# Kernel tuning notes

Hardware: AMD Instinct MI355X
Metric: run time of the kernel (lower is better)

## Reference

```python
import jax, jax.numpy as jnp
import numpy as np

N_NODES = 50000
NEG_SLOPE = 0.2


def _gat_conv(x, src, dst, W, a_src, a_dst, b, num_nodes):
    # W: [H*C, F_in]; a_src/a_dst: [H, C]; b: [H*C]
    H, C = a_src.shape
    xp = (x @ W.T).reshape(num_nodes, H, C)              # [N,H,C]
    alpha_s = jnp.sum(xp * a_src[None], axis=-1)          # [N,H]
    alpha_d = jnp.sum(xp * a_dst[None], axis=-1)          # [N,H]
    e = jax.nn.leaky_relu(alpha_s[src] + alpha_d[dst], NEG_SLOPE)  # [E,H]
    # segment softmax over incoming edges of each dst node (self-loops guarantee non-empty segments)
    m = jax.ops.segment_max(e, dst, num_segments=num_nodes)
    e = jnp.exp(e - m[dst])
    s = jax.ops.segment_sum(e, dst, num_segments=num_nodes)
    alpha = e / s[dst]                                    # [E,H]
    out = jax.ops.segment_sum(alpha[:, :, None] * xp[src], dst, num_segments=num_nodes)  # [N,H,C]
    return out.reshape(num_nodes, H * C) + b


def setup_inputs() -> dict:
    key = jax.random.key(0)
    ks = jax.random.split(key, 12)
    N, E, F_in, HID, H, Z = N_NODES, 800000, 128, 64, 2, 32
    sc = 0.1
    return {
        "features": jax.random.normal(ks[0], (N, F_in), jnp.float32),
        "edges": jax.random.randint(ks[1], (2, E), 0, N, jnp.int32),
        "W1": jax.random.normal(ks[2], (H * HID, F_in), jnp.float32) * sc,
        "a_src1": jax.random.normal(ks[3], (H, HID), jnp.float32) * sc,
        "a_dst1": jax.random.normal(ks[4], (H, HID), jnp.float32) * sc,
        "b1": jnp.zeros((H * HID,), jnp.float32),
        "W_mu": jax.random.normal(ks[5], (Z, H * HID), jnp.float32) * sc,
        "a_src_mu": jax.random.normal(ks[6], (1, Z), jnp.float32) * sc,
        "a_dst_mu": jax.random.normal(ks[7], (1, Z), jnp.float32) * sc,
        "b_mu": jnp.zeros((Z,), jnp.float32),
        "W_std": jax.random.normal(ks[8], (Z, H * HID), jnp.float32) * sc,
        "a_src_std": jax.random.normal(ks[9], (1, Z), jnp.float32) * sc,
        "a_dst_std": jax.random.normal(ks[10], (1, Z), jnp.float32) * sc,
        "b_std": jnp.zeros((Z,), jnp.float32),
    }


def reference(features, edges, W1, a_src1, a_dst1, b1, W_mu, a_src_mu, a_dst_mu, b_mu, W_std, a_src_std, a_dst_std, b_std):
    N = features.shape[0]
    loops = jnp.arange(N, dtype=edges.dtype)
    src = jnp.concatenate([edges[0], loops])  # add self loops (PyG default)
    dst = jnp.concatenate([edges[1], loops])
    h = _gat_conv(features, src, dst, W1, a_src1, a_dst1, b1, N)
    h = jax.nn.relu(h)  # dropout p=0.0 -> identity
    mu = _gat_conv(h, src, dst, W_mu, a_src_mu, a_dst_mu, b_mu, N)
    std = _gat_conv(h, src, dst, W_std, a_src_std, a_dst_std, b_std, N)
    return (mu, std)
```

## Files before the change

### kernel.cpp

```cpp
#include <hip/hip_runtime.h>
#include <math.h>

#define N_NODES 50000
#define N_EDGES 800000
#define ET (N_EDGES + N_NODES)
#define KD 128
#define Z 32
#define SH 7
#define BW 128
#define NBUCK ((N_NODES + BW - 1) / BW)
#define CHUNK 4096
#define NBLKA ((ET + CHUNK - 1) / CHUNK)
#define MTOT (NBUCK * NBLKA)
#define MBS ((MTOT + 1023) / 1024)
#define WCB 64

typedef __attribute__((ext_vector_type(8))) short bf16x8;
typedef __attribute__((ext_vector_type(4))) float f32x4;

static __device__ __forceinline__ float lrelu(float x){ return x > 0.f ? x : 0.2f*x; }
static __device__ __forceinline__ float lof(unsigned int u){ return __uint_as_float(u << 16); }
static __device__ __forceinline__ float hif(unsigned int u){ return __uint_as_float(u & 0xffff0000u); }
static __device__ __forceinline__ unsigned short f2bf(float f){
  unsigned int x = __float_as_uint(f);
  return (unsigned short)((x + 0x7fffu + ((x >> 16) & 1u)) >> 16);
}
static __device__ __forceinline__ unsigned int pack2(float lo, float hi){
  return (unsigned int)f2bf(lo) | ((unsigned int)f2bf(hi) << 16);
}

static __device__ __forceinline__ void bhistA_body(int k, const int* __restrict__ edges, int* __restrict__ M){
  int t = threadIdx.x;
  __shared__ int cnt[NBUCK];
  for(int b = t; b < NBUCK; b += 256) cnt[b] = 0;
  __syncthreads();
  int base = k*CHUNK;
  int lim = min(base + CHUNK, ET);
  for(int i = base + t; i < lim; i += 256){
    int d = (i < N_EDGES) ? edges[N_EDGES + i] : (i - N_EDGES);
    atomicAdd(&cnt[d >> SH], 1);
  }
  __syncthreads();
  for(int b = t; b < NBUCK; b += 256) M[b*NBLKA + k] = cnt[b];
}

static __device__ __forceinline__ void wconv_body(int bid, const float* __restrict__ W1,
                                                  const float* __restrict__ Wmu, const float* __restrict__ Wst,
                                                  unsigned short* __restrict__ Wb1, unsigned short* __restrict__ Wb2){
  int i = bid*256 + threadIdx.x;
  if(i < 128*KD) Wb1[i] = f2bf(W1[i]);
  if(i < 64*KD) Wb2[i] = f2bf(i < 32*KD ? Wmu[i] : Wst[i - 32*KD]);
}

__global__ __launch_bounds__(256) void packA_kernel(const int* __restrict__ edges, int* __restrict__ M,
                                                    const float* __restrict__ W1,
                                                    const float* __restrict__ Wmu, const float* __restrict__ Wst,
                                                    unsigned short* __restrict__ Wb1, unsigned short* __restrict__ Wb2){
  if(blockIdx.x < NBLKA) bhistA_body(blockIdx.x, edges, M);
  else                   wconv_body(blockIdx.x - NBLKA, W1, Wmu, Wst, Wb1, Wb2);
}

__global__ __launch_bounds__(256) void scanM1_kernel(const int* __restrict__ M, int* __restrict__ bsumM){
  int b = blockIdx.x, t = threadIdx.x;
  int base = b*1024 + t*4;
  int s = 0;
  #pragma unroll
  for(int i=0;i<4;i++){ int n = base+i; if(n < MTOT) s += M[n]; }
  for(int off=32; off; off>>=1) s += __shfl_xor(s, off);
  __shared__ int ws[4];
  if((t&63)==0) ws[t>>6] = s;
  __syncthreads();
  if(t==0) bsumM[b] = ws[0]+ws[1]+ws[2]+ws[3];
}

__global__ __launch_bounds__(256) void scanM2_kernel(const int* __restrict__ bsumM, int* __restrict__ bpreM){
  __shared__ int sm[256];
  int t = threadIdx.x;
  int v = (t < MBS) ? bsumM[t] : 0;
  sm[t] = v;
  __syncthreads();
  for(int off=1; off<256; off<<=1){
    int u = (t >= off) ? sm[t-off] : 0;
    __syncthreads();
    sm[t] += u;
    __syncthreads();
  }
  if(t < MBS) bpreM[t] = sm[t] - v;
}

__global__ __launch_bounds__(256) void scanM3_kernel(const int* __restrict__ M, const int* __restrict__ bpreM,
                                                     int* __restrict__ Mpos){
  int b = blockIdx.x, t = threadIdx.x;
  int lane = t & 63, wv = t >> 6;
  int base = b*1024 + t*4;
  int d[4]; int s = 0;
  #pragma unroll
  for(int i=0;i<4;i++){ int n = base+i; d[i] = (n < MTOT) ? M[n] : 0; s += d[i]; }
  int v = s;
  for(int off=1; off<64; off<<=1){
    int u = __shfl_up(v, off);
    if(lane >= off) v += u;
  }
  int texcl = v - s;
  __shared__ int wtot[4];
  if(lane == 63) wtot[wv] = v;
  __syncthreads();
  int woff = 0;
  for(int i=0;i<wv;i++) woff += wtot[i];
  int run = bpreM[b] + woff + texcl;
  #pragma unroll
  for(int i=0;i<4;i++){
    int n = base+i;
    if(n < MTOT){ Mpos[n] = run; run += d[i]; }
  }
}

static __device__ __forceinline__ void bplaceA_body(int k, const int* __restrict__ edges,
                                                    const int* __restrict__ Mpos, unsigned int* __restrict__ etmp){
  int t = threadIdx.x;
  __shared__ int cur[NBUCK];
  for(int b = t; b < NBUCK; b += 256) cur[b] = Mpos[b*NBLKA + k];
  __syncthreads();
  int base = k*CHUNK;
  int lim = min(base + CHUNK, ET);
  for(int i = base + t; i < lim; i += 256){
    int s, d;
    if(i < N_EDGES){ s = edges[i]; d = edges[N_EDGES+i]; } else { s = d = i - N_EDGES; }
    int pos = atomicAdd(&cur[d >> SH], 1);
    etmp[pos] = (unsigned int)s | ((unsigned int)(d & (BW-1)) << 17);
  }
}

static __device__ __forceinline__ void mmt1_body(int bid, const float* __restrict__ X,
                                                 const unsigned short* __restrict__ Wb,
                                                 const float* __restrict__ asv, const float* __restrict__ adv,
                                                 unsigned short* __restrict__ outb,
                                                 float* __restrict__ as1, float* __restrict__ ad1){
  constexpr int OC = 128, CT = 8;
  int t = threadIdx.x;
  int w = t >> 6, L = t & 63;
  int col = L & 15, quad = L >> 4;
  int row0 = bid*64 + w*16;
  int rA = row0 + col;
  if(rA >= N_NODES) rA = N_NODES-1;

  f32x4 acc[CT];
  #pragma unroll
  for(int ct=0;ct<CT;ct++) acc[ct] = (f32x4){0.f,0.f,0.f,0.f};

  #pragma unroll
  for(int kc=0;kc<4;kc++){
    int k0 = kc*32 + quad*8;
    const float* Xf = X + (size_t)rA*KD + k0;
    float4 p = *(const float4*)Xf;
    float4 q = *(const float4*)(Xf + 4);
    bf16x8 a;
    a[0] = (short)f2bf(p.x); a[1] = (short)f2bf(p.y);
    a[2] = (short)f2bf(p.z); a[3] = (short)f2bf(p.w);
    a[4] = (short)f2bf(q.x); a[5] = (short)f2bf(q.y);
    a[6] = (short)f2bf(q.z); a[7] = (short)f2bf(q.w);
    #pragma unroll
    for(int ct=0;ct<CT;ct++){
      bf16x8 b = *(const bf16x8*)(Wb + (size_t)(ct*16 + col)*KD + k0);
      acc[ct] = __builtin_amdgcn_mfma_f32_16x16x32_bf16(a, b, acc[ct], 0, 0, 0);
    }
  }

  float av[CT], dv[CT];
  #pragma unroll
  for(int ct=0;ct<CT;ct++){ av[ct] = asv[ct*16 + col]; dv[ct] = adv[ct*16 + col]; }

  #pragma unroll
  for(int r=0;r<4;r++){
    int row = row0 + quad*4 + r;
    #pragma unroll
    for(int ct=0;ct<CT;ct++)
      if(row < N_NODES) outb[(size_t)row*OC + ct*16 + col] = f2bf(acc[ct][r]);
    float s0 = acc[0][r]*av[0] + acc[1][r]*av[1] + acc[2][r]*av[2] + acc[3][r]*av[3];
    float s1 = acc[4][r]*av[4] + acc[5][r]*av[5] + acc[6][r]*av[6] + acc[7][r]*av[7];
    float d0 = acc[0][r]*dv[0] + acc[1][r]*dv[1] + acc[2][r]*dv[2] + acc[3][r]*dv[3];
    float d1 = acc[4][r]*dv[4] + acc[5][r]*dv[5] + acc[6][r]*dv[6] + acc[7][r]*dv[7];
    #pragma unroll
    for(int off=1; off<16; off<<=1){
      s0 += __shfl_xor(s0, off); s1 += __shfl_xor(s1, off);
      d0 += __shfl_xor(d0, off); d1 += __shfl_xor(d1, off);
    }
    if(col == 0 && row < N_NODES){
      as1[row*2] = s0; as1[row*2+1] = s1;
      ad1[row*2] = d0; ad1[row*2+1] = d1;
    }
  }
}

__global__ __launch_bounds__(256) void packB_kernel(const int* __restrict__ edges, const int* __restrict__ Mpos,
                                                    unsigned int* __restrict__ etmp,
                                                    const float* __restrict__ X, const unsigned short* __restrict__ Wb,
                                                    const float* __restrict__ asv, const float* __restrict__ adv,
                                                    unsigned short* __restrict__ outb,
                                                    float* __restrict__ as1, float* __restrict__ ad1){
  if(blockIdx.x < NBLKA) bplaceA_body(blockIdx.x, edges, Mpos, etmp);
  else                   mmt1_body(blockIdx.x - NBLKA, X, Wb, asv, adv, outb, as1, ad1);
}

__global__ __launch_bounds__(256) void bfin_kernel(const int* __restrict__ Mpos, const unsigned int* __restrict__ etmp,
                                                   int* __restrict__ rowptr, int* __restrict__ esrc,
                                                   int* __restrict__ edst){
  int b = blockIdx.x, t = threadIdx.x;
  __shared__ int cnt[BW];
  __shared__ int pre[BW];
  __shared__ int lcur[BW];
  if(t < BW) cnt[t] = 0;
  if(b == 0 && t < 32) esrc[ET + t] = 0;
  __syncthreads();
  int beg = Mpos[b*NBLKA];
  int end = (b+1 < NBUCK) ? Mpos[(b+1)*NBLKA] : ET;
  for(int i = beg + t; i < end; i += 256) atomicAdd(&cnt[etmp[i] >> 17], 1);
  __syncthreads();
  if(t < BW) pre[t] = cnt[t];
  __syncthreads();
  for(int off=1; off<BW; off<<=1){
    int u = 0;
    if(t < BW && t >= off) u = pre[t-off];
    __syncthreads();
    if(t < BW) pre[t] += u;
    __syncthreads();
  }
  if(t < BW){
    int excl = pre[t] - cnt[t];
    int node = b*BW + t;
    if(node < N_NODES) rowptr[node] = beg + excl;
    lcur[t] = beg + excl;
  }
  if(b == 0 && t == 255) rowptr[N_NODES] = ET;
  __syncthreads();
  for(int i = beg + t; i < end; i += 256){
    unsigned int e = etmp[i];
    int lo = (int)(e >> 17);
    int pos = atomicAdd(&lcur[lo], 1);
    esrc[pos] = (int)(e & 0x1FFFFu);
    edst[pos] = b*BW + lo;
  }
}

__global__ __launch_bounds__(256) void mmt2_kernel(const unsigned short* __restrict__ Xb,
                                                   const unsigned short* __restrict__ Wb,
                                                   const float* __restrict__ asmu, const float* __restrict__ admu,
                                                   const float* __restrict__ asst, const float* __restrict__ adst,
                                                   unsigned short* __restrict__ outb,
                                                   float* __restrict__ as2, float* __restrict__ ad2){
  constexpr int OC = 64, CT = 4;
  int t = threadIdx.x;
  int w = t >> 6, L = t & 63;
  int col = L & 15, quad = L >> 4;
  int row0 = blockIdx.x*64 + w*16;
  int rA = row0 + col;
  if(rA >= N_NODES) rA = N_NODES-1;

  f32x4 acc[CT];
  #pragma unroll
  for(int ct=0;ct<CT;ct++) acc[ct] = (f32x4){0.f,0.f,0.f,0.f};

  #pragma unroll
  for(int kc=0;kc<4;kc++){
    int k0 = kc*32 + quad*8;
    bf16x8 a = *(const bf16x8*)(Xb + (size_t)rA*KD + k0);
    #pragma unroll
    for(int ct=0;ct<CT;ct++){
      bf16x8 b = *(const bf16x8*)(Wb + (size_t)(ct*16 + col)*KD + k0);
      acc[ct] = __builtin_amdgcn_mfma_f32_16x16x32_bf16(a, b, acc[ct], 0, 0, 0);
    }
  }

  float av[CT], dv[CT];
  #pragma unroll
  for(int ct=0;ct<CT;ct++){
    av[ct] = (ct < 2) ? asmu[ct*16 + col] : asst[(ct-2)*16 + col];
    dv[ct] = (ct < 2) ? admu[ct*16 + col] : adst[(ct-2)*16 + col];
  }

  #pragma unroll
  for(int r=0;r<4;r++){
    int row = row0 + quad*4 + r;
    #pragma unroll
    for(int ct=0;ct<CT;ct++)
      if(row < N_NODES) outb[(size_t)row*OC + ct*16 + col] = f2bf(acc[ct][r]);
    float smu = acc[0][r]*av[0] + acc[1][r]*av[1];
    float sst = acc[2][r]*av[2] + acc[3][r]*av[3];
    float dmu = acc[0][r]*dv[0] + acc[1][r]*dv[1];
    float dst = acc[2][r]*dv[2] + acc[3][r]*dv[3];
    #pragma unroll
    for(int off=1; off<16; off<<=1){
      smu += __shfl_xor(smu, off); sst += __shfl_xor(sst, off);
      dmu += __shfl_xor(dmu, off); dst += __shfl_xor(dst, off);
    }
    if(col == 0 && row < N_NODES){
      as2[row*2] = smu; as2[row*2+1] = sst;
      ad2[row*2] = dmu; ad2[row*2+1] = dst;
    }
  }
}

__global__ __launch_bounds__(256) void wcalc_kernel(const int* __restrict__ esrc, const int* __restrict__ edst,
                                                    const float* __restrict__ as, const float* __restrict__ ad,
                                                    float2* __restrict__ wp){
  int i = blockIdx.x*256 + threadIdx.x;
  if(i >= ET) return;
  int s = esrc[i], d = edst[i];
  float2 a = ((const float2*)as)[s];
  float2 b = ((const float2*)ad)[d];
  wp[i] = make_float2(__expf(lrelu(a.x + b.x)), __expf(lrelu(a.y + b.y)));
}

__global__ __launch_bounds__(256) void agg1_kernel(const int* __restrict__ rowptr, const int* __restrict__ esrc,
                                                   const float2* __restrict__ wp,
                                                   const uint4* __restrict__ xb4,
                                                   const float* __restrict__ b1, uint4* __restrict__ hb4){
  int node = blockIdx.x*4 + (threadIdx.x>>6);
  int l = threadIdx.x & 63;
  if(node >= N_NODES) return;
  int g = l >> 4, c = l & 15;
  int beg = rowptr[node], end = rowptr[node+1];
  int n = end - beg;
  float a0=0.f,a1=0.f,a2=0.f,a3=0.f,a4=0.f,a5=0.f,a6=0.f,a7=0.f;
  float s0=0.f, s1=0.f;

#define S1_STEP(IDX) { \
    int e_ = esrc[(IDX)]; \
    float2 w_ = wp[(IDX)]; \
    uint4 u_ = xb4[(size_t)e_*16 + c]; \
    s0 += w_.x; s1 += w_.y; \
    float vv = (c < 8) ? w_.x : w_.y; \
    a0 += vv*lof(u_.x); a1 += vv*hif(u_.x); \
    a2 += vv*lof(u_.y); a3 += vv*hif(u_.y); \
    a4 += vv*lof(u_.z); a5 += vv*hif(u_.z); \
    a6 += vv*lof(u_.w); a7 += vv*hif(u_.w); }

#define S1_STEPM(IDX) { \
    int e_ = esrc[(IDX)]; \
    float2 w_ = wp[(IDX)]; \
    uint4 u_ = xb4[(size_t)e_*16 + c]; \
    float wx_ = ((IDX) < end) ? w_.x : 0.f; \
    float wy_ = ((IDX) < end) ? w_.y : 0.f; \
    s0 += wx_; s1 += wy_; \
    float vv = (c < 8) ? wx_ : wy_; \
    a0 += vv*lof(u_.x); a1 += vv*hif(u_.x); \
    a2 += vv*lof(u_.y); a3 += vv*hif(u_.y); \
    a4 += vv*lof(u_.z); a5 += vv*hif(u_.z); \
    a6 += vv*lof(u_.w); a7 += vv*hif(u_.w); }

  int i = beg;
  int nfull = n & ~7;
  for(; i < beg + nfull; i += 8){
    S1_STEP(i + g)
    S1_STEP(i + 4 + g)
  }
  if(i < end){
    S1_STEPM(i + g)
    S1_STEPM(i + 4 + g)
  }
#undef S1_STEP
#undef S1_STEPM

  #pragma unroll
  for(int off=16; off<64; off<<=1){
    s0 += __shfl_xor(s0,off); s1 += __shfl_xor(s1,off);
    a0 += __shfl_xor(a0,off); a1 += __shfl_xor(a1,off);
    a2 += __shfl_xor(a2,off); a3 += __shfl_xor(a3,off);
    a4 += __shfl_xor(a4,off); a5 += __shfl_xor(a5,off);
    a6 += __shfl_xor(a6,off); a7 += __shfl_xor(a7,off);
  }
  if(g == 0){
    float sd = (c < 8) ? s0 : s1;
    float inv = 1.f / sd;
    const float4* bp = (const float4*)(b1 + 8*c);
    float4 bl = bp[0], bh = bp[1];
    float r0 = fmaxf(a0*inv + bl.x, 0.f);
    float r1 = fmaxf(a1*inv + bl.y, 0.f);
    float r2 = fmaxf(a2*inv + bl.z, 0.f);
    float r3 = fmaxf(a3*inv + bl.w, 0.f);
    float r4 = fmaxf(a4*inv + bh.x, 0.f);
    float r5 = fmaxf(a5*inv + bh.y, 0.f);
    float r6 = fmaxf(a6*inv + bh.z, 0.f);
    float r7 = fmaxf(a7*inv + bh.w, 0.f);
    uint4 o;
    o.x = pack2(r0, r1); o.y = pack2(r2, r3);
    o.z = pack2(r4, r5); o.w = pack2(r6, r7);
    hb4[(size_t)node*16 + c] = o;
  }
}

__global__ __launch_bounds__(256) void agg2_kernel(const int* __restrict__ rowptr, const int* __restrict__ esrc,
                                                   const float2* __restrict__ wp,
                                                   const uint4* __restrict__ xb4,
                                                   const float* __restrict__ bmu, const float* __restrict__ bst,
                                                   float* __restrict__ out){
  int node = blockIdx.x*4 + (threadIdx.x>>6);
  int l = threadIdx.x & 63;
  if(node >= N_NODES) return;
  int g = l >> 3, c = l & 7;
  int beg = rowptr[node], end = rowptr[node+1];
  int n = end - beg;
  float a0=0.f,a1=0.f,a2=0.f,a3=0.f,a4=0.f,a5=0.f,a6=0.f,a7=0.f;
  float smu=0.f, sst=0.f;

#define S2_STEP(IDX) { \
    int e_ = esrc[(IDX)]; \
    float2 w_ = wp[(IDX)]; \
    uint4 u_ = xb4[(size_t)e_*8 + c]; \
    smu += w_.x; sst += w_.y; \
    float vv = (c < 4) ? w_.x : w_.y; \
    a0 += vv*lof(u_.x); a1 += vv*hif(u_.x); \
    a2 += vv*lof(u_.y); a3 += vv*hif(u_.y); \
    a4 += vv*lof(u_.z); a5 += vv*hif(u_.z); \
    a6 += vv*lof(u_.w); a7 += vv*hif(u_.w); }

#define S2_STEPM(IDX) { \
    int e_ = esrc[(IDX)]; \
    float2 w_ = wp[(IDX)]; \
    uint4 u_ = xb4[(size_t)e_*8 + c]; \
    float wx_ = ((IDX) < end) ? w_.x : 0.f; \
    float wy_ = ((IDX) < end) ? w_.y : 0.f; \
    smu += wx_; sst += wy_; \
    float vv = (c < 4) ? wx_ : wy_; \
    a0 += vv*lof(u_.x); a1 += vv*hif(u_.x); \
    a2 += vv*lof(u_.y); a3 += vv*hif(u_.y); \
    a4 += vv*lof(u_.z); a5 += vv*hif(u_.z); \
    a6 += vv*lof(u_.w); a7 += vv*hif(u_.w); }

  int i = beg;
  int nfull = n & ~15;
  for(; i < beg + nfull; i += 16){
    S2_STEP(i + g)
    S2_STEP(i + 8 + g)
  }
  if(i < end){
    S2_STEPM(i + g)
    S2_STEPM(i + 8 + g)
  }
#undef S2_STEP
#undef S2_STEPM

  #pragma unroll
  for(int off=8; off<64; off<<=1){
    smu += __shfl_xor(smu,off); sst += __shfl_xor(sst,off);
    a0 += __shfl_xor(a0,off); a1 += __shfl_xor(a1,off);
    a2 += __shfl_xor(a2,off); a3 += __shfl_xor(a3,off);
    a4 += __shfl_xor(a4,off); a5 += __shfl_xor(a5,off);
    a6 += __shfl_xor(a6,off); a7 += __shfl_xor(a7,off);
  }
  if(g == 0){
    float sd = (c < 4) ? smu : sst;
    float inv = 1.f / sd;
    const float* bb = (c < 4) ? (bmu + 8*c) : (bst + 8*(c-4));
    float4 bl = *(const float4*)bb;
    float4 bh = *(const float4*)(bb + 4);
    float* op = (c < 4) ? (out + (size_t)node*Z + 8*c)
                        : (out + (size_t)N_NODES*Z + (size_t)node*Z + 8*(c-4));
    float4 r0, r1;
    r0.x = a0*inv + bl.x; r0.y = a1*inv + bl.y;
    r0.z = a2*inv + bl.z; r0.w = a3*inv + bl.w;
    r1.x = a4*inv + bh.x; r1.y = a5*inv + bh.y;
    r1.z = a6*inv + bh.z; r1.w = a7*inv + bh.w;
    *(float4*)op = r0;
    *((float4*)op + 1) = r1;
  }
}

extern "C" void kernel_launch(void* const* d_in, const int* in_sizes, int n_in,
                              void* d_out, int out_size, void* d_ws, size_t ws_size,
                              hipStream_t stream){
  const float* x    = (const float*)d_in[0];
  const int*   edges= (const int*)d_in[1];
  const float* W1   = (const float*)d_in[2];
  const float* as1v = (const float*)d_in[3];
  const float* ad1v = (const float*)d_in[4];
  const float* b1   = (const float*)d_in[5];
  const float* Wmu  = (const float*)d_in[6];
  const float* asmu = (const float*)d_in[7];
  const float* admu = (const float*)d_in[8];
  const float* bmu  = (const float*)d_in[9];
  const float* Wst  = (const float*)d_in[10];
  const float* asst = (const float*)d_in[11];
  const float* adst = (const float*)d_in[12];
  const float* bst  = (const float*)d_in[13];
  float* out = (float*)d_out;

  char* p = (char*)d_ws;
  auto alloc = [&](size_t bytes)->char*{ char* r = p; p += (bytes + 255) & ~size_t(255); return r; };
  int*   M      = (int*)  alloc((size_t)MTOT*4);
  int*   Mpos   = (int*)  alloc((size_t)MTOT*4);
  int*   bsumM  = (int*)  alloc((size_t)MBS*4);
  int*   bpreM  = (int*)  alloc((size_t)MBS*4);
  unsigned int* etmp = (unsigned int*)alloc((size_t)ET*4);
  int*   esrc   = (int*)  alloc((size_t)(ET+32)*4);
  int*   edst   = (int*)  alloc((size_t)ET*4);
  int*   rowptr = (int*)  alloc((size_t)(N_NODES+1)*4);
  float2* wedge = (float2*)alloc((size_t)(ET+32)*8);
  unsigned short* Wb1 = (unsigned short*)alloc((size_t)128*KD*2);
  unsigned short* Wb2 = (unsigned short*)alloc((size_t)64*KD*2);
  unsigned short* xpb1 = (unsigned short*)alloc((size_t)N_NODES*128*2);
  float* as1    = (float*)alloc((size_t)N_NODES*2*4);
  float* ad1    = (float*)alloc((size_t)N_NODES*2*4);
  unsigned short* hb = (unsigned short*)alloc((size_t)N_NODES*128*2);
  float* as2    = (float*)alloc((size_t)N_NODES*2*4);
  float* ad2    = (float*)alloc((size_t)N_NODES*2*4);
  unsigned short* xpb2 = xpb1;

  packA_kernel  <<<NBLKA + WCB, 256, 0, stream>>>(edges, M, W1, Wmu, Wst, Wb1, Wb2);
  scanM1_kernel <<<MBS, 256, 0, stream>>>(M, bsumM);
  scanM2_kernel <<<1, 256, 0, stream>>>(bsumM, bpreM);
  scanM3_kernel <<<MBS, 256, 0, stream>>>(M, bpreM, Mpos);
  packB_kernel  <<<NBLKA + (N_NODES+63)/64, 256, 0, stream>>>(edges, Mpos, etmp,
                                                              x, Wb1, as1v, ad1v, xpb1, as1, ad1);
  bfin_kernel   <<<NBUCK, 256, 0, stream>>>(Mpos, etmp, rowptr, esrc, edst);

  wcalc_kernel <<<(ET+255)/256, 256, 0, stream>>>(esrc, edst, as1, ad1, wedge);
  agg1_kernel  <<<(N_NODES+3)/4, 256, 0, stream>>>(rowptr, esrc, wedge, (const uint4*)xpb1, b1, (uint4*)hb);

  mmt2_kernel  <<<(N_NODES+63)/64, 256, 0, stream>>>(hb, Wb2, asmu, admu, asst, adst, xpb1, as2, ad2);
  wcalc_kernel <<<(ET+255)/256, 256, 0, stream>>>(esrc, edst, as2, ad2, wedge);
  agg2_kernel  <<<(N_NODES+3)/4, 256, 0, stream>>>(rowptr, esrc, wedge, (const uint4*)xpb2, bmu, bst, out);
}
```

Before: 227.0 us.

## Fuse scan stages, edge-weight calc into CSR build, and layer-2 attention logits into agg1

Merges the two top-level scan kernels into one by having each block reduce the preceding block sums itself. Computes layer-1 edge weights inside the CSR finalize kernel, which already has the source and destination of each edge. Precomputes W^T·a vectors for the second layer so that agg1 produces the layer-2 attention logits directly from the fp32 activations. This lets the second matmul and its edge-weight pass run together in one launch. The aim is to remove several kernel launches and extra passes over the edge arrays, at the cost of more work in agg1 and a change in rounding, since the logits now come from fp32 rather than bf16-rounded products.

```diff
diff --git a/kernel.cpp b/kernel.cpp
--- a/kernel.cpp
+++ b/kernel.cpp
@@ -14,6 +14,8 @@
 #define MTOT (NBUCK * NBLKA)
 #define MBS ((MTOT + 1023) / 1024)
 #define WCB 64
+#define MM2B ((N_NODES + 63) / 64)
+#define WCE ((ET + 255) / 256)
 
 typedef __attribute__((ext_vector_type(8))) short bf16x8;
 typedef __attribute__((ext_vector_type(4))) float f32x4;
@@ -52,12 +54,32 @@
   if(i < 64*KD) Wb2[i] = f2bf(i < 32*KD ? Wmu[i] : Wst[i - 32*KD]);
 }
 
+static __device__ __forceinline__ void vacalc_body(const float* __restrict__ Wmu, const float* __restrict__ Wst,
+                                                   const float* __restrict__ asmu, const float* __restrict__ admu,
+                                                   const float* __restrict__ asst, const float* __restrict__ adst,
+                                                   float* __restrict__ va){
+  int k = threadIdx.x;
+  if(k >= 128) return;
+  float smu = 0.f, dmu = 0.f, sst = 0.f, dst = 0.f;
+  #pragma unroll 8
+  for(int z = 0; z < Z; z++){
+    float wm = Wmu[z*128 + k], ws = Wst[z*128 + k];
+    smu += asmu[z]*wm; dmu += admu[z]*wm;
+    sst += asst[z]*ws; dst += adst[z]*ws;
+  }
+  va[k] = smu; va[128 + k] = dmu; va[256 + k] = sst; va[384 + k] = dst;
+}
+
 __global__ __launch_bounds__(256) void packA_kernel(const int* __restrict__ edges, int* __restrict__ M,
                                                     const float* __restrict__ W1,
                                                     const float* __restrict__ Wmu, const float* __restrict__ Wst,
-                                                    unsigned short* __restrict__ Wb1, unsigned short* __restrict__ Wb2){
-  if(blockIdx.x < NBLKA) bhistA_body(blockIdx.x, edges, M);
-  else                   wconv_body(blockIdx.x - NBLKA, W1, Wmu, Wst, Wb1, Wb2);
+                                                    unsigned short* __restrict__ Wb1, unsigned short* __restrict__ Wb2,
+                                                    const float* __restrict__ asmu, const float* __restrict__ admu,
+                                                    const float* __restrict__ asst, const float* __restrict__ adst,
+                                                    float* __restrict__ va){
+  if(blockIdx.x < NBLKA)            bhistA_body(blockIdx.x, edges, M);
+  else if(blockIdx.x < NBLKA + WCB) wconv_body(blockIdx.x - NBLKA, W1, Wmu, Wst, Wb1, Wb2);
+  else                              vacalc_body(Wmu, Wst, asmu, admu, asst, adst, va);
 }
 
 __global__ __launch_bounds__(256) void scanM1_kernel(const int* __restrict__ M, int* __restrict__ bsumM){
@@ -73,25 +95,16 @@
   if(t==0) bsumM[b] = ws[0]+ws[1]+ws[2]+ws[3];
 }
 
-__global__ __launch_bounds__(256) void scanM2_kernel(const int* __restrict__ bsumM, int* __restrict__ bpreM){
-  __shared__ int sm[256];
-  int t = threadIdx.x;
-  int v = (t < MBS) ? bsumM[t] : 0;
-  sm[t] = v;
-  __syncthreads();
-  for(int off=1; off<256; off<<=1){
-    int u = (t >= off) ? sm[t-off] : 0;
-    __syncthreads();
-    sm[t] += u;
-    __syncthreads();
-  }
-  if(t < MBS) bpreM[t] = sm[t] - v;
-}
-
-__global__ __launch_bounds__(256) void scanM3_kernel(const int* __restrict__ M, const int* __restrict__ bpreM,
-                                                     int* __restrict__ Mpos){
+__global__ __launch_bounds__(256) void scanM23_kernel(const int* __restrict__ M, const int* __restrict__ bsumM,
+                                                      int* __restrict__ Mpos){
   int b = blockIdx.x, t = threadIdx.x;
   int lane = t & 63, wv = t >> 6;
+  __shared__ int wsum[4];
+  int pv = (t < b && t < MBS) ? bsumM[t] : 0;
+  for(int off=32; off; off>>=1) pv += __shfl_xor(pv, off);
+  if(lane == 0) wsum[wv] = pv;
+  __syncthreads();
+  int bpre = wsum[0] + wsum[1] + wsum[2] + wsum[3];
   int base = b*1024 + t*4;
   int d[4]; int s = 0;
   #pragma unroll
@@ -107,7 +120,7 @@
   __syncthreads();
   int woff = 0;
   for(int i=0;i<wv;i++) woff += wtot[i];
-  int run = bpreM[b] + woff + texcl;
+  int run = bpre + woff + texcl;
   #pragma unroll
   for(int i=0;i<4;i++){
     int n = base+i;
@@ -204,12 +217,19 @@
 
 __global__ __launch_bounds__(256) void bfin_kernel(const int* __restrict__ Mpos, const unsigned int* __restrict__ etmp,
                                                    int* __restrict__ rowptr, int* __restrict__ esrc,
-                                                   int* __restrict__ edst){
+                                                   int* __restrict__ edst,
+                                                   const float* __restrict__ as1, const float* __restrict__ ad1,
+                                                   float2* __restrict__ wp){
   int b = blockIdx.x, t = threadIdx.x;
   __shared__ int cnt[BW];
   __shared__ int pre[BW];
   __shared__ int lcur[BW];
-  if(t < BW) cnt[t] = 0;
+  __shared__ float2 adl[BW];
+  if(t < BW){
+    cnt[t] = 0;
+    int node = b*BW + t;
+    adl[t] = (node < N_NODES) ? ((const float2*)ad1)[node] : make_float2(0.f, 0.f);
+  }
   if(b == 0 && t < 32) esrc[ET + t] = 0;
   __syncthreads();
   int beg = Mpos[b*NBLKA];
@@ -233,26 +253,28 @@
   }
   if(b == 0 && t == 255) rowptr[N_NODES] = ET;
   __syncthreads();
+  const float2* asp = (const float2*)as1;
   for(int i = beg + t; i < end; i += 256){
     unsigned int e = etmp[i];
     int lo = (int)(e >> 17);
+    int s  = (int)(e & 0x1FFFFu);
     int pos = atomicAdd(&lcur[lo], 1);
-    esrc[pos] = (int)(e & 0x1FFFFu);
+    esrc[pos] = s;
     edst[pos] = b*BW + lo;
-  }
-}
-
-__global__ __launch_bounds__(256) void mmt2_kernel(const unsigned short* __restrict__ Xb,
-                                                   const unsigned short* __restrict__ Wb,
-                                                   const float* __restrict__ asmu, const float* __restrict__ admu,
-                                                   const float* __restrict__ asst, const float* __restrict__ adst,
-                                                   unsigned short* __restrict__ outb,
-                                                   float* __restrict__ as2, float* __restrict__ ad2){
+    float2 a = asp[s];
+    float2 dd = adl[lo];
+    wp[pos] = make_float2(__expf(lrelu(a.x + dd.x)), __expf(lrelu(a.y + dd.y)));
+  }
+}
+
+static __device__ __forceinline__ void mmt2_body(int bid, const unsigned short* __restrict__ Xb,
+                                                 const unsigned short* __restrict__ Wb,
+                                                 unsigned short* __restrict__ outb){
   constexpr int OC = 64, CT = 4;
   int t = threadIdx.x;
   int w = t >> 6, L = t & 63;
   int col = L & 15, quad = L >> 4;
-  int row0 = blockIdx.x*64 + w*16;
+  int row0 = bid*64 + w*16;
   int rA = row0 + col;
   if(rA >= N_NODES) rA = N_NODES-1;
 
@@ -271,39 +293,19 @@
     }
   }
 
-  float av[CT], dv[CT];
-  #pragma unroll
-  for(int ct=0;ct<CT;ct++){
-    av[ct] = (ct < 2) ? asmu[ct*16 + col] : asst[(ct-2)*16 + col];
-    dv[ct] = (ct < 2) ? admu[ct*16 + col] : adst[(ct-2)*16 + col];
-  }
-
   #pragma unroll
   for(int r=0;r<4;r++){
     int row = row0 + quad*4 + r;
     #pragma unroll
     for(int ct=0;ct<CT;ct++)
       if(row < N_NODES) outb[(size_t)row*OC + ct*16 + col] = f2bf(acc[ct][r]);
-    float smu = acc[0][r]*av[0] + acc[1][r]*av[1];
-    float sst = acc[2][r]*av[2] + acc[3][r]*av[3];
-    float dmu = acc[0][r]*dv[0] + acc[1][r]*dv[1];
-    float dst = acc[2][r]*dv[2] + acc[3][r]*dv[3];
-    #pragma unroll
-    for(int off=1; off<16; off<<=1){
-      smu += __shfl_xor(smu, off); sst += __shfl_xor(sst, off);
-      dmu += __shfl_xor(dmu, off); dst += __shfl_xor(dst, off);
-    }
-    if(col == 0 && row < N_NODES){
-      as2[row*2] = smu; as2[row*2+1] = sst;
-      ad2[row*2] = dmu; ad2[row*2+1] = dst;
-    }
-  }
-}
-
-__global__ __launch_bounds__(256) void wcalc_kernel(const int* __restrict__ esrc, const int* __restrict__ edst,
-                                                    const float* __restrict__ as, const float* __restrict__ ad,
-                                                    float2* __restrict__ wp){
-  int i = blockIdx.x*256 + threadIdx.x;
+  }
+}
+
+static __device__ __forceinline__ void wcalc_body(int bid, const int* __restrict__ esrc, const int* __restrict__ edst,
+                                                  const float* __restrict__ as, const float* __restrict__ ad,
+                                                  float2* __restrict__ wp){
+  int i = bid*256 + threadIdx.x;
   if(i >= ET) return;
   int s = esrc[i], d = edst[i];
   float2 a = ((const float2*)as)[s];
@@ -311,10 +313,22 @@
   wp[i] = make_float2(__expf(lrelu(a.x + b.x)), __expf(lrelu(a.y + b.y)));
 }
 
+__global__ __launch_bounds__(256) void packC_kernel(const unsigned short* __restrict__ Xb,
+                                                    const unsigned short* __restrict__ Wb,
+                                                    unsigned short* __restrict__ outb,
+                                                    const int* __restrict__ esrc, const int* __restrict__ edst,
+                                                    const float* __restrict__ as2, const float* __restrict__ ad2,
+                                                    float2* __restrict__ wp){
+  if(blockIdx.x < MM2B) mmt2_body(blockIdx.x, Xb, Wb, outb);
+  else                  wcalc_body(blockIdx.x - MM2B, esrc, edst, as2, ad2, wp);
+}
+
 __global__ __launch_bounds__(256) void agg1_kernel(const int* __restrict__ rowptr, const int* __restrict__ esrc,
                                                    const float2* __restrict__ wp,
                                                    const uint4* __restrict__ xb4,
-                                                   const float* __restrict__ b1, uint4* __restrict__ hb4){
+                                                   const float* __restrict__ b1, uint4* __restrict__ hb4,
+                                                   const float* __restrict__ va,
+                                                   float* __restrict__ as2, float* __restrict__ ad2){
   int node = blockIdx.x*4 + (threadIdx.x>>6);
   int l = threadIdx.x & 63;
   if(node >= N_NODES) return;
@@ -369,23 +383,42 @@
     a4 += __shfl_xor(a4,off); a5 += __shfl_xor(a5,off);
     a6 += __shfl_xor(a6,off); a7 += __shfl_xor(a7,off);
   }
+  float sd = (c < 8) ? s0 : s1;
+  float inv = 1.f / sd;
+  const float4* bp = (const float4*)(b1 + 8*c);
+  float4 bl = bp[0], bh = bp[1];
+  float r0 = fmaxf(a0*inv + bl.x, 0.f);
+  float r1 = fmaxf(a1*inv + bl.y, 0.f);
+  float r2 = fmaxf(a2*inv + bl.z, 0.f);
+  float r3 = fmaxf(a3*inv + bl.w, 0.f);
+  float r4 = fmaxf(a4*inv + bh.x, 0.f);
+  float r5 = fmaxf(a5*inv + bh.y, 0.f);
+  float r6 = fmaxf(a6*inv + bh.z, 0.f);
+  float r7 = fmaxf(a7*inv + bh.w, 0.f);
   if(g == 0){
-    float sd = (c < 8) ? s0 : s1;
-    float inv = 1.f / sd;
-    const float4* bp = (const float4*)(b1 + 8*c);
-    float4 bl = bp[0], bh = bp[1];
-    float r0 = fmaxf(a0*inv + bl.x, 0.f);
-    float r1 = fmaxf(a1*inv + bl.y, 0.f);
-    float r2 = fmaxf(a2*inv + bl.z, 0.f);
-    float r3 = fmaxf(a3*inv + bl.w, 0.f);
-    float r4 = fmaxf(a4*inv + bh.x, 0.f);
-    float r5 = fmaxf(a5*inv + bh.y, 0.f);
-    float r6 = fmaxf(a6*inv + bh.z, 0.f);
-    float r7 = fmaxf(a7*inv + bh.w, 0.f);
     uint4 o;
     o.x = pack2(r0, r1); o.y = pack2(r2, r3);
     o.z = pack2(r4, r5); o.w = pack2(r6, r7);
     hb4[(size_t)node*16 + c] = o;
+  }
+  const float4* v0 = (const float4*)(va +        8*c);
+  const float4* v1 = (const float4*)(va + 128 +  8*c);
+  const float4* v2 = (const float4*)(va + 256 +  8*c);
+  const float4* v3 = (const float4*)(va + 384 +  8*c);
+  float4 m0 = v0[0], m1 = v0[1], d0v = v1[0], d1v = v1[1];
+  float4 t0 = v2[0], t1 = v2[1], u0 = v3[0], u1 = v3[1];
+  float psmu = r0*m0.x + r1*m0.y + r2*m0.z + r3*m0.w + r4*m1.x + r5*m1.y + r6*m1.z + r7*m1.w;
+  float pdmu = r0*d0v.x + r1*d0v.y + r2*d0v.z + r3*d0v.w + r4*d1v.x + r5*d1v.y + r6*d1v.z + r7*d1v.w;
+  float psst = r0*t0.x + r1*t0.y + r2*t0.z + r3*t0.w + r4*t1.x + r5*t1.y + r6*t1.z + r7*t1.w;
+  float pdst = r0*u0.x + r1*u0.y + r2*u0.z + r3*u0.w + r4*u1.x + r5*u1.y + r6*u1.z + r7*u1.w;
+  #pragma unroll
+  for(int off=1; off<16; off<<=1){
+    psmu += __shfl_xor(psmu, off); pdmu += __shfl_xor(pdmu, off);
+    psst += __shfl_xor(psst, off); pdst += __shfl_xor(pdst, off);
+  }
+  if(l == 0){
+    as2[node*2] = psmu; as2[node*2+1] = psst;
+    ad2[node*2] = pdmu; ad2[node*2+1] = pdst;
   }
 }
 
@@ -490,12 +523,12 @@
   int*   M      = (int*)  alloc((size_t)MTOT*4);
   int*   Mpos   = (int*)  alloc((size_t)MTOT*4);
   int*   bsumM  = (int*)  alloc((size_t)MBS*4);
-  int*   bpreM  = (int*)  alloc((size_t)MBS*4);
   unsigned int* etmp = (unsigned int*)alloc((size_t)ET*4);
   int*   esrc   = (int*)  alloc((size_t)(ET+32)*4);
   int*   edst   = (int*)  alloc((size_t)ET*4);
   int*   rowptr = (int*)  alloc((size_t)(N_NODES+1)*4);
   float2* wedge = (float2*)alloc((size_t)(ET+32)*8);
+  float* va     = (float*)alloc((size_t)512*4);
   unsigned short* Wb1 = (unsigned short*)alloc((size_t)128*KD*2);
   unsigned short* Wb2 = (unsigned short*)alloc((size_t)64*KD*2);
   unsigned short* xpb1 = (unsigned short*)alloc((size_t)N_NODES*128*2);
@@ -506,18 +539,16 @@
   float* ad2    = (float*)alloc((size_t)N_NODES*2*4);
   unsigned short* xpb2 = xpb1;
 
-  packA_kernel  <<<NBLKA + WCB, 256, 0, stream>>>(edges, M, W1, Wmu, Wst, Wb1, Wb2);
+  packA_kernel  <<<NBLKA + WCB + 1, 256, 0, stream>>>(edges, M, W1, Wmu, Wst, Wb1, Wb2,
+                                                      asmu, admu, asst, adst, va);
   scanM1_kernel <<<MBS, 256, 0, stream>>>(M, bsumM);
-  scanM2_kernel <<<1, 256, 0, stream>>>(bsumM, bpreM);
-  scanM3_kernel <<<MBS, 256, 0, stream>>>(M, bpreM, Mpos);
-  packB_kernel  <<<NBLKA + (N_NODES+63)/64, 256, 0, stream>>>(edges, Mpos, etmp,
-                                                              x, Wb1, as1v, ad1v, xpb1, as1, ad1);
-  bfin_kernel   <<<NBUCK, 256, 0, stream>>>(Mpos, etmp, rowptr, esrc, edst);
-
-  wcalc_kernel <<<(ET+255)/256, 256, 0, stream>>>(esrc, edst, as1, ad1, wedge);
-  agg1_kernel  <<<(N_NODES+3)/4, 256, 0, stream>>>(rowptr, esrc, wedge, (const uint4*)xpb1, b1, (uint4*)hb);
-
-  mmt2_kernel  <<<(N_NODES+63)/64, 256, 0, stream>>>(hb, Wb2, asmu, admu, asst, adst, xpb1, as2, ad2);
-  wcalc_kernel <<<(ET+255)/256, 256, 0, stream>>>(esrc, edst, as2, ad2, wedge);
+  scanM23_kernel<<<MBS, 256, 0, stream>>>(M, bsumM, Mpos);
+  packB_kernel  <<<NBLKA + MM2B, 256, 0, stream>>>(edges, Mpos, etmp,
+                                                   x, Wb1, as1v, ad1v, xpb1, as1, ad1);
+  bfin_kernel   <<<NBUCK, 256, 0, stream>>>(Mpos, etmp, rowptr, esrc, edst, as1, ad1, wedge);
+
+  agg1_kernel  <<<(N_NODES+3)/4, 256, 0, stream>>>(rowptr, esrc, wedge, (const uint4*)xpb1, b1, (uint4*)hb,
+                                                   va, as2, ad2);
+  packC_kernel <<<MM2B + WCE, 256, 0, stream>>>(hb, Wb2, xpb1, esrc, edst, as2, ad2, wedge);
   agg2_kernel  <<<(N_NODES+3)/4, 256, 0, stream>>>(rowptr, esrc, wedge, (const uint4*)xpb2, bmu, bst, out);
 }
```

After: 225.6 us. About the same (-0.6%).
